# Performance work log

Hardware: AMD Instinct MI355X
Metric: run time of the kernel (lower is better)

The kernel has to match this reference:

```python
import jax, jax.numpy as jnp
import numpy as np

B, N, FEAT, HID, H = 4, 2048, 512, 512, 8
HD = HID // H  # head_dim = 64


def rotate_half(x):
    # pairs along last dim: (x1, x2) -> (-x2, x1), interleaved
    x = x.reshape(*x.shape[:-1], -1, 2)
    x1, x2 = x[..., 0], x[..., 1]
    return jnp.stack((-x2, x1), axis=-1).reshape(*x.shape[:-2], -1)


def apply_rope(freqs, t):
    # freqs: [2, B, 1, N, HD] broadcasting over heads; t: [B, H, N, HD]
    return t * freqs[0] + rotate_half(t) * freqs[1]


def setup_inputs() -> dict:
    key = jax.random.key(0)
    ks = jax.random.split(key, 12)
    s = 0.02
    return {
        "x0": jax.random.normal(ks[0], (B, N, FEAT), jnp.float32),
        "x1": jax.random.normal(ks[1], (B, N, FEAT), jnp.float32),
        "encoding0": jax.random.normal(ks[2], (2, B, 1, N, HD), jnp.float32),
        "encoding1": jax.random.normal(ks[3], (2, B, 1, N, HD), jnp.float32),
        "Wqkv": jax.random.normal(ks[4], (FEAT, 3 * HID), jnp.float32) * s,
        "bqkv": jnp.zeros((3 * HID,), jnp.float32),
        "Wproj": jax.random.normal(ks[5], (HID, HID), jnp.float32) * s,
        "bproj": jnp.zeros((HID,), jnp.float32),
        "W1": jax.random.normal(ks[6], (FEAT + HID, 2 * FEAT), jnp.float32) * s,
        "b1": jnp.zeros((2 * FEAT,), jnp.float32),
        "ln_g": jnp.ones((2 * FEAT,), jnp.float32),
        "ln_b": jnp.zeros((2 * FEAT,), jnp.float32),
        "W2": jax.random.normal(ks[7], (2 * FEAT, FEAT), jnp.float32) * s,
        "b2": jnp.zeros((FEAT,), jnp.float32),
    }


def _block(x, enc, Wqkv, bqkv, Wproj, bproj, W1, b1, ln_g, ln_b, W2, b2):
    b, n, _ = x.shape
    qkv = x @ Wqkv + bqkv                                   # [B,N,3*HID]
    qkv = qkv.reshape(b, n, H, HD, 3).transpose(0, 2, 1, 3, 4)  # [B,H,N,HD,3]
    q, k, v = qkv[..., 0], qkv[..., 1], qkv[..., 2]
    q = apply_rope(enc, q)
    k = apply_rope(enc, k)
    scale = q.shape[-1] ** (-0.5)
    attn = jax.nn.softmax(jnp.einsum('bhid,bhjd->bhij', q, k) * scale, axis=-1)
    o = jnp.einsum('bhij,bhjd->bhid', attn, v)              # [B,H,N,HD]
    message = o.transpose(0, 2, 1, 3).reshape(b, n, HID) @ Wproj + bproj
    h = jnp.concatenate([x, message], axis=-1) @ W1 + b1    # [B,N,2*FEAT]
    mu = h.mean(-1, keepdims=True)
    var = ((h - mu) ** 2).mean(-1, keepdims=True)
    h = (h - mu) * jax.lax.rsqrt(var + 1e-5) * ln_g + ln_b
    return x + jax.nn.gelu(h, approximate=False) @ W2 + b2


def reference(x0, x1, encoding0, encoding1, Wqkv, bqkv, Wproj, bproj, W1, b1, ln_g, ln_b, W2, b2):
    p = (Wqkv, bqkv, Wproj, bproj, W1, b1, ln_g, ln_b, W2, b2)
    return (_block(x0, encoding0, *p), _block(x1, encoding1, *p))
```

## Files before the change

kernel.cpp:

```cpp
#include <hip/hip_runtime.h>
#include <hip/hip_bf16.h>

typedef __attribute__((ext_vector_type(8))) short   short8v;
typedef __attribute__((ext_vector_type(4))) short   short4v;
typedef __attribute__((ext_vector_type(8))) __bf16  bf16x8;
typedef __attribute__((ext_vector_type(4))) __bf16  bf16x4;
typedef __attribute__((ext_vector_type(4))) float   f32x4;

constexpr int Nn = 2048;

#define GLOAD_LDS(src, dst) \
  __builtin_amdgcn_global_load_lds((__attribute__((address_space(1))) unsigned int*)(src), \
                                   (__attribute__((address_space(3))) unsigned int*)(dst), 16, 0, 0)

#if __has_builtin(__builtin_amdgcn_exp2f)
#define EXP2F(x) __builtin_amdgcn_exp2f(x)
#else
#define EXP2F(x) exp2f(x)
#endif

#if __has_builtin(__builtin_amdgcn_mfma_f32_16x16x16bf16_1k)
#define HAVE_MFMA16 1
#define MFMA16(a, b, c) __builtin_amdgcn_mfma_f32_16x16x16bf16_1k(a, b, c, 0, 0, 0)
#else
#define HAVE_MFMA16 0
#endif

__device__ __forceinline__ unsigned pack_bf16(float lo, float hi) {
  union { __bf16 h[2]; unsigned u; } t;
  t.h[0] = (__bf16)lo; t.h[1] = (__bf16)hi;
  return t.u;
}

template<int AMODE, int BMODE, int EPI>
__global__ __launch_bounds__(256)
void gemm_mfma(const __bf16* __restrict__ A, const __bf16* __restrict__ A2,
               const __bf16* __restrict__ BT, const __bf16* __restrict__ BT2,
               const float* __restrict__ bias,
               const float* __restrict__ resid0, const float* __restrict__ resid1,
               float* __restrict__ Cf, __bf16* __restrict__ Cb, __bf16* __restrict__ Vt,
               int lda, int ldb, int ldb2, int ldc, int K1, int K)
{
  __shared__ __align__(16) __bf16 As[2][4096];
  __shared__ __align__(16) __bf16 Bs[2][4096];
  const int tid = threadIdx.x;
  const int w = tid >> 6, l = tid & 63;
  const int wr = w >> 1, wc = w & 1;
  const int lr = l & 15, lg = l >> 4;
  const int row0 = blockIdx.x * 128, col0 = blockIdx.y * 128;

  f32x4 acc[4][4];
#pragma unroll
  for (int i = 0; i < 4; ++i)
#pragma unroll
    for (int j = 0; j < 4; ++j) acc[i][j] = (f32x4){0.f, 0.f, 0.f, 0.f};

  const int srow = l >> 2;
  const int skk  = (l & 3) * 8;

  auto stage = [&](int k0, int b) {
#pragma unroll
    for (int s = w; s < 8; s += 4) {
      const int m = s * 16 + srow;
      const __bf16* src;
      if constexpr (AMODE == 0) {
        src = A + (size_t)(row0 + m) * lda + k0 + skk;
      } else {
        const int gk = k0 + skk;
        src = (gk < K1) ? A  + (size_t)(row0 + m) * lda + gk
                        : A2 + (size_t)(row0 + m) * lda + (gk - K1);
      }
      GLOAD_LDS(src, &As[b][s * 512]);
    }
#pragma unroll
    for (int s = w; s < 8; s += 4) {
      const int n = s * 16 + srow;
      const __bf16* src;
      if constexpr (BMODE == 0) {
        src = BT + (size_t)(col0 + n) * ldb + k0 + skk;
      } else {
        const int gk = k0 + skk;
        src = (gk < K1) ? BT  + (size_t)(col0 + n) * ldb + gk
                        : BT2 + (size_t)(col0 + n) * ldb2 + (gk - K1);
      }
      GLOAD_LDS(src, &Bs[b][s * 512]);
    }
  };

  const int nt = K >> 5;
  stage(0, 0);

  for (int t = 0; t < nt; ++t) {
    const int p = t & 1;
    if (t + 1 < nt) {
      stage((t + 1) * 32, 1 - p);
      asm volatile("s_waitcnt vmcnt(4)" ::: "memory");
    } else {
      asm volatile("s_waitcnt vmcnt(0)" ::: "memory");
    }
    __builtin_amdgcn_sched_barrier(0);
    __builtin_amdgcn_s_barrier();
    __builtin_amdgcn_sched_barrier(0);
    bf16x8 af[4], bfv[4];
#pragma unroll
    for (int mi = 0; mi < 4; ++mi)
      af[mi] = *(const bf16x8*)&As[p][(wr * 64 + mi * 16 + lr) * 32 + lg * 8];
#pragma unroll
    for (int ni = 0; ni < 4; ++ni)
      bfv[ni] = *(const bf16x8*)&Bs[p][(wc * 64 + ni * 16 + lr) * 32 + lg * 8];
    __builtin_amdgcn_s_setprio(1);
#pragma unroll
    for (int mi = 0; mi < 4; ++mi)
#pragma unroll
      for (int ni = 0; ni < 4; ++ni)
        acc[mi][ni] = __builtin_amdgcn_mfma_f32_16x16x32_bf16(af[mi], bfv[ni], acc[mi][ni], 0, 0, 0);
    __builtin_amdgcn_s_setprio(0);
    __builtin_amdgcn_s_barrier();
  }

  if constexpr (EPI == 4) {
    if (col0 >= 1024) {
      const int b2 = row0 >> 11;
#pragma unroll
      for (int mi = 0; mi < 4; ++mi)
#pragma unroll
        for (int ni = 0; ni < 4; ++ni) {
          const int col = col0 + wc * 64 + ni * 16 + lr;
          const int sec = col - 1024, h = sec >> 6, d = sec & 63;
          const int n0 = (row0 + wr * 64 + mi * 16 + lg * 4) & 2047;
          union { __bf16 h4[4]; short4 s4; } u;
#pragma unroll
          for (int r = 0; r < 4; ++r) u.h4[r] = (__bf16)(acc[mi][ni][r] + bias[col]);
          *(short4*)&Vt[(size_t)(b2 * 8 + h) * 131072 + (size_t)d * 2048 + n0] = u.s4;
        }
    } else {
#pragma unroll
      for (int mi = 0; mi < 4; ++mi)
#pragma unroll
        for (int ni = 0; ni < 4; ++ni) {
          const int col = col0 + wc * 64 + ni * 16 + lr;
#pragma unroll
          for (int r = 0; r < 4; ++r) {
            const int row = row0 + wr * 64 + mi * 16 + lg * 4 + r;
            Cb[(size_t)row * 1024 + col] = (__bf16)(acc[mi][ni][r] + bias[col]);
          }
        }
    }
    return;
  }

#pragma unroll
  for (int mi = 0; mi < 4; ++mi)
#pragma unroll
    for (int ni = 0; ni < 4; ++ni) {
      const int col = col0 + wc * 64 + ni * 16 + lr;
#pragma unroll
      for (int r = 0; r < 4; ++r) {
        const int row = row0 + wr * 64 + mi * 16 + lg * 4 + r;
        const float v = acc[mi][ni][r];
        if constexpr (EPI == 1) {
          Cb[(size_t)row * ldc + col] = (__bf16)(v + bias[col]);
        } else if constexpr (EPI == 3) {
          Cb[(size_t)row * ldc + col] = (__bf16)v;
        } else {
          const float* rp = (row < 8192) ? resid0 : resid1;
          Cf[(size_t)row * ldc + col] = v + bias[col] + rp[(size_t)(row & 8191) * ldc + col];
        }
      }
    }
}

__global__ __launch_bounds__(256, 2)
void fa_k(const __bf16* __restrict__ QK, const __bf16* __restrict__ Vg,
          __bf16* __restrict__ Ob)
{
  __shared__ __align__(16) __bf16 Ks[2][8192];
  __shared__ __align__(16) __bf16 Vs[2][8192];
  const int tid = threadIdx.x;
  const int w = tid >> 6, l = tid & 63;
  const int lr = l & 15, lg = l >> 4;
  const int bh = blockIdx.y;
  const int b2 = bh >> 3, h = bh & 7;
  const __bf16* Qp = QK + (size_t)b2 * 2048 * 1024 + h * 64;
  const __bf16* Kp = Qp + 512;
  const __bf16* Vp = Vg + (size_t)bh * 131072;
  const int q0 = blockIdx.x * 128 + w * 32;

  bf16x8 qf[2][2];
#pragma unroll
  for (int nf = 0; nf < 2; ++nf)
#pragma unroll
    for (int kk = 0; kk < 2; ++kk)
      qf[nf][kk] = *(const bf16x8*)&Qp[(size_t)(q0 + nf * 16 + lr) * 1024 + kk * 32 + lg * 8];

  f32x4 oacc[4][2];
#pragma unroll
  for (int i = 0; i < 4; ++i)
#pragma unroll
    for (int j = 0; j < 2; ++j) oacc[i][j] = (f32x4){0.f, 0.f, 0.f, 0.f};
  float m_run[2] = {-1e30f, -1e30f}, lsum[2] = {0.f, 0.f};

#if !HAVE_MFMA16
  const int Sa = (lg & 1) * 32 + lr, Sb2x = Sa + 16;
  const bool hi = (lg >> 1) & 1;
#endif

  auto stage = [&](int kv0, int b) {
#pragma unroll
    for (int i = 0; i < 4; ++i) {
      const int s = w + 4 * i;
      { const int g = s * 64 + l, r = g >> 3, c = g & 7;
        GLOAD_LDS(Kp + (size_t)(kv0 + r) * 1024 + ((c ^ (r & 7)) * 8), &Ks[b][s * 512]); }
      { const int g = s * 64 + l, r = g >> 4, c = g & 15;
        GLOAD_LDS(Vp + (size_t)r * 2048 + kv0 + ((c ^ (r & 15)) * 8), &Vs[b][s * 512]); }
    }
  };

  stage(0, 0);

  for (int t = 0; t < 16; ++t) {
    const int p = t & 1;
    if (t < 15) {
      stage((t + 1) * 128, 1 - p);
      asm volatile("s_waitcnt vmcnt(8)" ::: "memory");
    } else {
      asm volatile("s_waitcnt vmcnt(0)" ::: "memory");
    }
    __builtin_amdgcn_sched_barrier(0);
    __builtin_amdgcn_s_barrier();
    __builtin_amdgcn_sched_barrier(0);

    f32x4 sacc[8][2];
#pragma unroll
    for (int i = 0; i < 8; ++i)
#pragma unroll
      for (int j = 0; j < 2; ++j) sacc[i][j] = (f32x4){0.f, 0.f, 0.f, 0.f};
#pragma unroll
    for (int kk = 0; kk < 2; ++kk) {
      bf16x8 ka[8];
#pragma unroll
      for (int mf = 0; mf < 8; ++mf)
        ka[mf] = *(const bf16x8*)&Ks[p][(mf * 16 + lr) * 64 + (((kk * 4 + lg) ^ (lr & 7)) * 8)];
      __builtin_amdgcn_s_setprio(1);
#pragma unroll
      for (int mf = 0; mf < 8; ++mf)
#pragma unroll
        for (int nf = 0; nf < 2; ++nf)
          sacc[mf][nf] = __builtin_amdgcn_mfma_f32_16x16x32_bf16(ka[mf], qf[nf][kk], sacc[mf][nf], 0, 0, 0);
      __builtin_amdgcn_s_setprio(0);
    }

    unsigned pkk[8][2][2];
#pragma unroll
    for (int nf = 0; nf < 2; ++nf) {
      float tm = -1e30f;
#pragma unroll
      for (int mf = 0; mf < 8; ++mf)
#pragma unroll
        for (int r = 0; r < 4; ++r) tm = fmaxf(tm, sacc[mf][nf][r]);
      tm = fmaxf(tm, __shfl_xor(tm, 16, 64));
      tm = fmaxf(tm, __shfl_xor(tm, 32, 64));
      if (__any(tm > m_run[nf] + 8.f)) {
        const float mn = fmaxf(m_run[nf], tm);
        const float corr = EXP2F(m_run[nf] - mn);
        m_run[nf] = mn;
        lsum[nf] *= corr;
#pragma unroll
        for (int mo = 0; mo < 4; ++mo)
#pragma unroll
          for (int r = 0; r < 4; ++r) oacc[mo][nf][r] *= corr;
      }
      const float mcur = m_run[nf];
      float rs = 0.f;
#pragma unroll
      for (int mf = 0; mf < 8; ++mf) {
        const float p0 = EXP2F(sacc[mf][nf][0] - mcur);
        const float p1 = EXP2F(sacc[mf][nf][1] - mcur);
        const float p2 = EXP2F(sacc[mf][nf][2] - mcur);
        const float p3 = EXP2F(sacc[mf][nf][3] - mcur);
        rs += (p0 + p1) + (p2 + p3);
        pkk[mf][nf][0] = pack_bf16(p0, p1);
        pkk[mf][nf][1] = pack_bf16(p2, p3);
      }
      rs += __shfl_xor(rs, 16, 64);
      rs += __shfl_xor(rs, 32, 64);
      lsum[nf] += rs;
    }

#if HAVE_MFMA16
#pragma unroll
    for (int ks = 0; ks < 8; ++ks) {
      bf16x4 va[4];
#pragma unroll
      for (int mo = 0; mo < 4; ++mo) {
        const int og = 2 * ks + (lg >> 1);
        va[mo] = *(const bf16x4*)&Vs[p][(mo * 16 + lr) * 128 + ((og ^ lr) & 15) * 8 + (lg & 1) * 4];
      }
      __builtin_amdgcn_s_setprio(1);
#pragma unroll
      for (int mo = 0; mo < 4; ++mo)
#pragma unroll
        for (int nf = 0; nf < 2; ++nf)
          oacc[mo][nf] = MFMA16(__builtin_bit_cast(short4v, va[mo]),
                                __builtin_bit_cast(short4v, pkk[ks][nf]),
                                oacc[mo][nf]);
      __builtin_amdgcn_s_setprio(0);
    }
#else
#pragma unroll
    for (int kf = 0; kf < 4; ++kf) {
      bf16x8 va[4];
#pragma unroll
      for (int mo = 0; mo < 4; ++mo)
        va[mo] = *(const bf16x8*)&Vs[p][(mo * 16 + lr) * 128 + ((((kf * 4 + lg) ^ lr) & 15) * 8)];
      bf16x8 bfr[2];
#pragma unroll
      for (int nf = 0; nf < 2; ++nf) {
        const unsigned s0 = hi ? pkk[kf * 2 + 1][nf][0] : pkk[kf * 2][nf][0];
        const unsigned s1 = hi ? pkk[kf * 2 + 1][nf][1] : pkk[kf * 2][nf][1];
        union { unsigned u[4]; bf16x8 v; } ub;
        ub.u[0] = (unsigned)__shfl((int)s0, Sa, 64);
        ub.u[1] = (unsigned)__shfl((int)s1, Sa, 64);
        ub.u[2] = (unsigned)__shfl((int)s0, Sb2x, 64);
        ub.u[3] = (unsigned)__shfl((int)s1, Sb2x, 64);
        bfr[nf] = ub.v;
      }
      __builtin_amdgcn_s_setprio(1);
#pragma unroll
      for (int mo = 0; mo < 4; ++mo)
#pragma unroll
        for (int nf = 0; nf < 2; ++nf)
          oacc[mo][nf] = __builtin_amdgcn_mfma_f32_16x16x32_bf16(va[mo], bfr[nf], oacc[mo][nf], 0, 0, 0);
      __builtin_amdgcn_s_setprio(0);
    }
#endif
    __builtin_amdgcn_s_barrier();
  }

#pragma unroll
  for (int nf = 0; nf < 2; ++nf) {
    const float inv = 1.f / lsum[nf];
    const long row = (long)b2 * 2048 + q0 + nf * 16 + lr;
#pragma unroll
    for (int mo = 0; mo < 4; ++mo) {
      union { __bf16 h4[4]; short4 s4; } u;
#pragma unroll
      for (int r = 0; r < 4; ++r) u.h4[r] = (__bf16)(oacc[mo][nf][r] * inv);
      *(short4*)&Ob[row * 512 + h * 64 + mo * 16 + lg * 4] = u.s4;
    }
  }
}

__global__ __launch_bounds__(256)
void conv_f32_bf16_k(const float* __restrict__ s, __bf16* __restrict__ d)
{
  const long i = ((long)blockIdx.x * 256 + threadIdx.x) * 4;
  const float4 v = *(const float4*)&s[i];
  union { __bf16 h[4]; short4 sv; } u;
  u.h[0] = (__bf16)v.x; u.h[1] = (__bf16)v.y; u.h[2] = (__bf16)v.z; u.h[3] = (__bf16)v.w;
  *(short4*)&d[i] = u.sv;
}

template<int PERM>
__global__ __launch_bounds__(256)
void transpose_wt_k(const float* __restrict__ W, __bf16* __restrict__ WT, int K, int N)
{
  __shared__ float t[32][33];
  const int n0 = blockIdx.x * 32, k0 = blockIdx.y * 32;
  const int tx = threadIdx.x & 31, ty = threadIdx.x >> 5;
  for (int i = ty; i < 32; i += 8)
    t[i][tx] = W[(size_t)(k0 + i) * N + n0 + tx];
  __syncthreads();
  for (int i = ty; i < 32; i += 8) {
    int drow = n0 + i;
    if constexpr (PERM) {
      const int h = drow / 192, rem = drow % 192;
      drow = (rem % 3) * 512 + h * 64 + rem / 3;
    }
    WT[(size_t)drow * K + k0 + tx] = (__bf16)t[tx][i];
  }
}

__global__ void bperm_k(const float* __restrict__ b, float* __restrict__ bp)
{
  const int i = blockIdx.x * 256 + threadIdx.x;
  if (i < 1536) {
    const int h = i / 192, rem = i % 192;
    bp[(rem % 3) * 512 + h * 64 + rem / 3] = b[i];
  }
}

__global__ __launch_bounds__(256)
void bfuse_k(const float* __restrict__ b1, const float* __restrict__ bproj,
             const float* __restrict__ W1, float* __restrict__ b1f)
{
  const int n = blockIdx.x * 256 + threadIdx.x;
  float s = b1[n];
  for (int m = 0; m < 512; ++m)
    s += bproj[m] * W1[(size_t)(512 + m) * 1024 + n];
  b1f[n] = s;
}

__global__ __launch_bounds__(256)
void rope_k(__bf16* __restrict__ qkvb, const float* __restrict__ enc0,
            const float* __restrict__ enc1)
{
  constexpr float SCQ = 0.125f * 1.44269504089f;
  const long idx = (long)blockIdx.x * 256 + threadIdx.x;
  const int t = (int)(idx & 31);
  const int h = (int)((idx >> 5) & 7);
  const long row = idx >> 8;
  const long bn = row & 8191;
  const float* e = (row < 8192) ? enc0 : enc1;
  const int d0 = 2 * t;
  const float f0a = e[bn * 64 + d0], f0b = e[bn * 64 + d0 + 1];
  const float f1a = e[524288 + bn * 64 + d0], f1b = e[524288 + bn * 64 + d0 + 1];
  const long base = row * 1024 + (long)h * 64 + d0;
  {
    union { __bf16 hx[2]; unsigned u; } p;
    p.u = *(unsigned*)&qkvb[base];
    const float x0 = (float)p.hx[0], x1 = (float)p.hx[1];
    p.hx[0] = (__bf16)((x0 * f0a - x1 * f1a) * SCQ);
    p.hx[1] = (__bf16)((x1 * f0b + x0 * f1b) * SCQ);
    *(unsigned*)&qkvb[base] = p.u;
  }
  {
    union { __bf16 hx[2]; unsigned u; } p;
    p.u = *(unsigned*)&qkvb[base + 512];
    const float x0 = (float)p.hx[0], x1 = (float)p.hx[1];
    p.hx[0] = (__bf16)(x0 * f0a - x1 * f1a);
    p.hx[1] = (__bf16)(x1 * f0b + x0 * f1b);
    *(unsigned*)&qkvb[base + 512] = p.u;
  }
}

__global__ __launch_bounds__(256)
void ln_gelu_k(__bf16* __restrict__ Hb, const float* __restrict__ g,
               const float* __restrict__ be)
{
  __bf16* row = Hb + (size_t)blockIdx.x * 1024;
  const int tid = threadIdx.x;
  __shared__ float rs_[256], rq_[256];
  union { __bf16 h[4]; short4 sv; } u;
  u.sv = *(const short4*)&row[tid * 4];
  float v[4];
  float s = 0.f, sq = 0.f;
#pragma unroll
  for (int i = 0; i < 4; ++i) {
    v[i] = (float)u.h[i];
    s += v[i]; sq += v[i] * v[i];
  }
  rs_[tid] = s; rq_[tid] = sq; __syncthreads();
  for (int st = 128; st > 0; st >>= 1) {
    if (tid < st) { rs_[tid] += rs_[tid + st]; rq_[tid] += rq_[tid + st]; }
    __syncthreads();
  }
  const float mu = rs_[0] * (1.f / 1024.f);
  const float var = rq_[0] * (1.f / 1024.f) - mu * mu;
  const float rstd = rsqrtf(var + 1e-5f);
#pragma unroll
  for (int i = 0; i < 4; ++i) {
    const int c = tid * 4 + i;
    const float y = (v[i] - mu) * rstd * g[c] + be[c];
    u.h[i] = (__bf16)(0.5f * y * (1.f + erff(y * 0.70710678118f)));
  }
  *(short4*)&row[tid * 4] = u.sv;
}

extern "C" void kernel_launch(void* const* d_in, const int* in_sizes, int n_in,
                              void* d_out, int out_size, void* d_ws, size_t ws_size,
                              hipStream_t stream)
{
  const float* x0   = (const float*)d_in[0];
  const float* x1   = (const float*)d_in[1];
  const float* enc0 = (const float*)d_in[2];
  const float* enc1 = (const float*)d_in[3];
  const float* Wqkv  = (const float*)d_in[4];
  const float* bqkv  = (const float*)d_in[5];
  const float* Wproj = (const float*)d_in[6];
  const float* bproj = (const float*)d_in[7];
  const float* W1    = (const float*)d_in[8];
  const float* b1    = (const float*)d_in[9];
  const float* ln_g  = (const float*)d_in[10];
  const float* ln_b  = (const float*)d_in[11];
  const float* W2    = (const float*)d_in[12];
  const float* b2    = (const float*)d_in[13];

  __bf16* wsb = (__bf16*)d_ws;
  __bf16* xb      = wsb;
  __bf16* WqkvT   = wsb + 8388608;
  __bf16* Wproj_b = wsb + 9175040;
  __bf16* W1T     = wsb + 9437184;
  __bf16* W2T     = wsb + 10485760;
  float*  bqkvp   = (float*)(wsb + 11010048);
  __bf16* qkvb    = wsb + 11013120;
  __bf16* Vt      = wsb + 27790336;
  __bf16* Ob      = wsb + 36178944;
  __bf16* WfT     = wsb + 44567552;
  float*  b1f     = (float*)(wsb + 45091840);
  __bf16* hb      = qkvb;

  transpose_wt_k<1><<<dim3(48, 16), 256, 0, stream>>>(Wqkv, WqkvT, 512, 1536);
  transpose_wt_k<0><<<dim3(32, 32), 256, 0, stream>>>(W1, W1T, 1024, 1024);
  transpose_wt_k<0><<<dim3(16, 32), 256, 0, stream>>>(W2, W2T, 1024, 512);
  bperm_k<<<6, 256, 0, stream>>>(bqkv, bqkvp);
  conv_f32_bf16_k<<<256, 256, 0, stream>>>(Wproj, Wproj_b);
  gemm_mfma<0, 0, 3><<<dim3(8, 4), 256, 0, stream>>>(
      W1T + 512, nullptr, Wproj_b, nullptr, nullptr, nullptr, nullptr,
      nullptr, WfT, nullptr, 1024, 512, 0, 512, 0, 512);
  bfuse_k<<<4, 256, 0, stream>>>(b1, bproj, W1, b1f);

  conv_f32_bf16_k<<<4096, 256, 0, stream>>>(x0, xb);
  conv_f32_bf16_k<<<4096, 256, 0, stream>>>(x1, xb + 4194304);

  gemm_mfma<0, 0, 4><<<dim3(128, 12), 256, 0, stream>>>(
      xb, nullptr, WqkvT, nullptr, bqkvp, nullptr, nullptr, nullptr, qkvb, Vt,
      512, 512, 0, 1024, 0, 512);
  rope_k<<<16384, 256, 0, stream>>>(qkvb, enc0, enc1);
  fa_k<<<dim3(16, 64), 256, 0, stream>>>(qkvb, Vt, Ob);
  gemm_mfma<1, 1, 1><<<dim3(128, 8), 256, 0, stream>>>(
      xb, Ob, W1T, WfT, b1f, nullptr, nullptr, nullptr, hb, nullptr,
      512, 1024, 512, 1024, 512, 1024);
  ln_gelu_k<<<16384, 256, 0, stream>>>(hb, ln_g, ln_b);
  gemm_mfma<0, 0, 2><<<dim3(128, 4), 256, 0, stream>>>(
      hb, nullptr, W2T, nullptr, b2, x0, x1, (float*)d_out, nullptr, nullptr,
      1024, 1024, 0, 512, 0, 1024);
}
```

Measured before the change: 346.0 us.

## Fuse RoPE into QKV GEMM epilogue and shrink attention KV tiles

RoPE and the Q scaling move into the QKV GEMM epilogue, using a lane shuffle to fetch the paired element, so the separate rope kernel and its read-modify-write pass over Q/K disappear. The flash-attention kernel now processes 64-key tiles instead of 128, which halves its LDS footprint and changes the V swizzle to match. Its grid is flattened to 1D with a remapped block-to-(head, query tile) order, presumably to improve L2 locality or XCD distribution. Smaller KV tiles mean more loop iterations and barriers, and the epilogue now does extra scattered encoding loads per element.

```diff
diff --git a/kernel.cpp b/kernel.cpp
--- a/kernel.cpp
+++ b/kernel.cpp
@@ -134,15 +134,25 @@
           *(short4*)&Vt[(size_t)(b2 * 8 + h) * 131072 + (size_t)d * 2048 + n0] = u.s4;
         }
     } else {
+      constexpr float SCQ = 0.125f * 1.44269504089f;
+      const float* e = (row0 < 8192) ? resid0 : resid1;
 #pragma unroll
       for (int mi = 0; mi < 4; ++mi)
 #pragma unroll
         for (int ni = 0; ni < 4; ++ni) {
           const int col = col0 + wc * 64 + ni * 16 + lr;
+          const int d = col & 63;
+          const float sgn = (col & 1) ? 1.f : -1.f;
+          const float scq = (col < 512) ? SCQ : 1.f;
 #pragma unroll
           for (int r = 0; r < 4; ++r) {
             const int row = row0 + wr * 64 + mi * 16 + lg * 4 + r;
-            Cb[(size_t)row * 1024 + col] = (__bf16)(acc[mi][ni][r] + bias[col]);
+            const long bn = row & 8191;
+            const float f0 = e[bn * 64 + d];
+            const float f1 = e[524288 + bn * 64 + d];
+            const float vb = acc[mi][ni][r] + bias[col];
+            const float pb = __shfl_xor(vb, 1, 64);
+            Cb[(size_t)row * 1024 + col] = (__bf16)((vb * f0 + sgn * pb * f1) * scq);
           }
         }
     }
@@ -174,17 +184,19 @@
 void fa_k(const __bf16* __restrict__ QK, const __bf16* __restrict__ Vg,
           __bf16* __restrict__ Ob)
 {
-  __shared__ __align__(16) __bf16 Ks[2][8192];
-  __shared__ __align__(16) __bf16 Vs[2][8192];
+  __shared__ __align__(16) __bf16 Ks[2][4096];
+  __shared__ __align__(16) __bf16 Vs[2][4096];
   const int tid = threadIdx.x;
   const int w = tid >> 6, l = tid & 63;
   const int lr = l & 15, lg = l >> 4;
-  const int bh = blockIdx.y;
+  const int bid = blockIdx.x;
+  const int qi = (bid >> 3) & 15;
+  const int bh = (bid & 7) * 8 + (bid >> 7);
   const int b2 = bh >> 3, h = bh & 7;
   const __bf16* Qp = QK + (size_t)b2 * 2048 * 1024 + h * 64;
   const __bf16* Kp = Qp + 512;
   const __bf16* Vp = Vg + (size_t)bh * 131072;
-  const int q0 = blockIdx.x * 128 + w * 32;
+  const int q0 = qi * 128 + w * 32;
 
   bf16x8 qf[2][2];
 #pragma unroll
@@ -207,22 +219,21 @@
 
   auto stage = [&](int kv0, int b) {
 #pragma unroll
-    for (int i = 0; i < 4; ++i) {
+    for (int i = 0; i < 2; ++i) {
       const int s = w + 4 * i;
-      { const int g = s * 64 + l, r = g >> 3, c = g & 7;
-        GLOAD_LDS(Kp + (size_t)(kv0 + r) * 1024 + ((c ^ (r & 7)) * 8), &Ks[b][s * 512]); }
-      { const int g = s * 64 + l, r = g >> 4, c = g & 15;
-        GLOAD_LDS(Vp + (size_t)r * 2048 + kv0 + ((c ^ (r & 15)) * 8), &Vs[b][s * 512]); }
+      const int g = s * 64 + l, r = g >> 3, c = g & 7;
+      GLOAD_LDS(Kp + (size_t)(kv0 + r) * 1024 + ((c ^ (r & 7)) * 8), &Ks[b][s * 512]);
+      GLOAD_LDS(Vp + (size_t)r * 2048 + kv0 + ((c ^ (r & 7)) * 8), &Vs[b][s * 512]);
     }
   };
 
   stage(0, 0);
 
-  for (int t = 0; t < 16; ++t) {
+  for (int t = 0; t < 32; ++t) {
     const int p = t & 1;
-    if (t < 15) {
-      stage((t + 1) * 128, 1 - p);
-      asm volatile("s_waitcnt vmcnt(8)" ::: "memory");
+    if (t < 31) {
+      stage((t + 1) * 64, 1 - p);
+      asm volatile("s_waitcnt vmcnt(4)" ::: "memory");
     } else {
       asm volatile("s_waitcnt vmcnt(0)" ::: "memory");
     }
@@ -230,32 +241,32 @@
     __builtin_amdgcn_s_barrier();
     __builtin_amdgcn_sched_barrier(0);
 
-    f32x4 sacc[8][2];
-#pragma unroll
-    for (int i = 0; i < 8; ++i)
+    f32x4 sacc[4][2];
+#pragma unroll
+    for (int i = 0; i < 4; ++i)
 #pragma unroll
       for (int j = 0; j < 2; ++j) sacc[i][j] = (f32x4){0.f, 0.f, 0.f, 0.f};
 #pragma unroll
     for (int kk = 0; kk < 2; ++kk) {
-      bf16x8 ka[8];
-#pragma unroll
-      for (int mf = 0; mf < 8; ++mf)
+      bf16x8 ka[4];
+#pragma unroll
+      for (int mf = 0; mf < 4; ++mf)
         ka[mf] = *(const bf16x8*)&Ks[p][(mf * 16 + lr) * 64 + (((kk * 4 + lg) ^ (lr & 7)) * 8)];
       __builtin_amdgcn_s_setprio(1);
 #pragma unroll
-      for (int mf = 0; mf < 8; ++mf)
+      for (int mf = 0; mf < 4; ++mf)
 #pragma unroll
         for (int nf = 0; nf < 2; ++nf)
           sacc[mf][nf] = __builtin_amdgcn_mfma_f32_16x16x32_bf16(ka[mf], qf[nf][kk], sacc[mf][nf], 0, 0, 0);
       __builtin_amdgcn_s_setprio(0);
     }
 
-    unsigned pkk[8][2][2];
+    unsigned pkk[4][2][2];
 #pragma unroll
     for (int nf = 0; nf < 2; ++nf) {
       float tm = -1e30f;
 #pragma unroll
-      for (int mf = 0; mf < 8; ++mf)
+      for (int mf = 0; mf < 4; ++mf)
 #pragma unroll
         for (int r = 0; r < 4; ++r) tm = fmaxf(tm, sacc[mf][nf][r]);
       tm = fmaxf(tm, __shfl_xor(tm, 16, 64));
@@ -273,7 +284,7 @@
       const float mcur = m_run[nf];
       float rs = 0.f;
 #pragma unroll
-      for (int mf = 0; mf < 8; ++mf) {
+      for (int mf = 0; mf < 4; ++mf) {
         const float p0 = EXP2F(sacc[mf][nf][0] - mcur);
         const float p1 = EXP2F(sacc[mf][nf][1] - mcur);
         const float p2 = EXP2F(sacc[mf][nf][2] - mcur);
@@ -289,12 +300,12 @@
 
 #if HAVE_MFMA16
 #pragma unroll
-    for (int ks = 0; ks < 8; ++ks) {
+    for (int ks = 0; ks < 4; ++ks) {
       bf16x4 va[4];
 #pragma unroll
       for (int mo = 0; mo < 4; ++mo) {
-        const int og = 2 * ks + (lg >> 1);
-        va[mo] = *(const bf16x4*)&Vs[p][(mo * 16 + lr) * 128 + ((og ^ lr) & 15) * 8 + (lg & 1) * 4];
+        const int g = (ks * 2 + (lg >> 1)) ^ (lr & 7);
+        va[mo] = *(const bf16x4*)&Vs[p][(mo * 16 + lr) * 64 + g * 8 + (lg & 1) * 4];
       }
       __builtin_amdgcn_s_setprio(1);
 #pragma unroll
@@ -308,11 +319,13 @@
     }
 #else
 #pragma unroll
-    for (int kf = 0; kf < 4; ++kf) {
+    for (int kf = 0; kf < 2; ++kf) {
       bf16x8 va[4];
 #pragma unroll
-      for (int mo = 0; mo < 4; ++mo)
-        va[mo] = *(const bf16x8*)&Vs[p][(mo * 16 + lr) * 128 + ((((kf * 4 + lg) ^ lr) & 15) * 8)];
+      for (int mo = 0; mo < 4; ++mo) {
+        const int g = ((kf * 4 + lg) ^ (lr & 7));
+        va[mo] = *(const bf16x8*)&Vs[p][(mo * 16 + lr) * 64 + g * 8];
+      }
       bf16x8 bfr[2];
 #pragma unroll
       for (int nf = 0; nf < 2; ++nf) {
@@ -399,39 +412,6 @@
   for (int m = 0; m < 512; ++m)
     s += bproj[m] * W1[(size_t)(512 + m) * 1024 + n];
   b1f[n] = s;
-}
-
-__global__ __launch_bounds__(256)
-void rope_k(__bf16* __restrict__ qkvb, const float* __restrict__ enc0,
-            const float* __restrict__ enc1)
-{
-  constexpr float SCQ = 0.125f * 1.44269504089f;
-  const long idx = (long)blockIdx.x * 256 + threadIdx.x;
-  const int t = (int)(idx & 31);
-  const int h = (int)((idx >> 5) & 7);
-  const long row = idx >> 8;
-  const long bn = row & 8191;
-  const float* e = (row < 8192) ? enc0 : enc1;
-  const int d0 = 2 * t;
-  const float f0a = e[bn * 64 + d0], f0b = e[bn * 64 + d0 + 1];
-  const float f1a = e[524288 + bn * 64 + d0], f1b = e[524288 + bn * 64 + d0 + 1];
-  const long base = row * 1024 + (long)h * 64 + d0;
-  {
-    union { __bf16 hx[2]; unsigned u; } p;
-    p.u = *(unsigned*)&qkvb[base];
-    const float x0 = (float)p.hx[0], x1 = (float)p.hx[1];
-    p.hx[0] = (__bf16)((x0 * f0a - x1 * f1a) * SCQ);
-    p.hx[1] = (__bf16)((x1 * f0b + x0 * f1b) * SCQ);
-    *(unsigned*)&qkvb[base] = p.u;
-  }
-  {
-    union { __bf16 hx[2]; unsigned u; } p;
-    p.u = *(unsigned*)&qkvb[base + 512];
-    const float x0 = (float)p.hx[0], x1 = (float)p.hx[1];
-    p.hx[0] = (__bf16)(x0 * f0a - x1 * f1a);
-    p.hx[1] = (__bf16)(x1 * f0b + x0 * f1b);
-    *(unsigned*)&qkvb[base + 512] = p.u;
-  }
 }
 
 __global__ __launch_bounds__(256)
@@ -514,10 +494,9 @@
   conv_f32_bf16_k<<<4096, 256, 0, stream>>>(x1, xb + 4194304);
 
   gemm_mfma<0, 0, 4><<<dim3(128, 12), 256, 0, stream>>>(
-      xb, nullptr, WqkvT, nullptr, bqkvp, nullptr, nullptr, nullptr, qkvb, Vt,
+      xb, nullptr, WqkvT, nullptr, bqkvp, enc0, enc1, nullptr, qkvb, Vt,
       512, 512, 0, 1024, 0, 512);
-  rope_k<<<16384, 256, 0, stream>>>(qkvb, enc0, enc1);
-  fa_k<<<dim3(16, 64), 256, 0, stream>>>(qkvb, Vt, Ob);
+  fa_k<<<1024, 256, 0, stream>>>(qkvb, Vt, Ob);
   gemm_mfma<1, 1, 1><<<dim3(128, 8), 256, 0, stream>>>(
       xb, Ob, W1T, WfT, b1f, nullptr, nullptr, nullptr, hb, nullptr,
       512, 1024, 512, 1024, 512, 1024);
```

Measured after the change: 339.7 us. Within noise of the previous version (-1.8%).
